# Performance work log

Measured on AMD Instinct MI355X. Metric: run time of the kernel, lower is better.

Reference implementation:

```python
import jax, jax.numpy as jnp
import numpy as np

N_NODES, N_EDGES, D_IN, N_GRAPHS = 20000, 320000, 256, 32
H1, C1, H2, C2 = 4, 128, 4, 64


def setup_inputs() -> dict:
    key = jax.random.key(0)
    ks = jax.random.split(key, 24)
    g = lambda k, shape, fan: jax.random.normal(k, shape, jnp.float32) * (1.0 / np.sqrt(fan))
    inp = {
        'x': jax.random.normal(ks[0], (N_NODES, D_IN), jnp.float32),
        'edge_index': jax.random.randint(ks[1], (2, N_EDGES), 0, N_NODES, jnp.int32),
        'batch': jnp.sort(jax.random.randint(ks[2], (N_NODES,), 0, N_GRAPHS, jnp.int32)),
        'edge_attr': jax.random.normal(ks[3], (N_EDGES, 1), jnp.float32),
        # GATConv 1: lin [D_IN, H1*C1], att_src/dst/edge [H1,C1], lin_edge [1,H1*C1], bias [H1*C1]
        'W1': g(ks[4], (D_IN, H1 * C1), D_IN),
        'as1': g(ks[5], (H1, C1), C1),
        'ad1': g(ks[6], (H1, C1), C1),
        'We1': g(ks[7], (1, H1 * C1), 1),
        'ae1': g(ks[8], (H1, C1), C1),
        'b1': jnp.zeros((H1 * C1,), jnp.float32),
        'g1': jnp.ones((H1 * C1,), jnp.float32),
        'be1': jnp.zeros((H1 * C1,), jnp.float32),
        # GATConv 2 (concat=False -> out 64)
        'W2': g(ks[9], (H1 * C1, H2 * C2), H1 * C1),
        'as2': g(ks[10], (H2, C2), C2),
        'ad2': g(ks[11], (H2, C2), C2),
        'We2': g(ks[12], (1, H2 * C2), 1),
        'ae2': g(ks[13], (H2, C2), C2),
        'b2': jnp.zeros((C2,), jnp.float32),
        'g2': jnp.ones((C2,), jnp.float32),
        'be2': jnp.zeros((C2,), jnp.float32),
        'fw1': g(ks[14], (C2, 32), C2),
        'fb1': jnp.zeros((32,), jnp.float32),
        'fw2': g(ks[15], (32, 1), 32),
        'fb2': jnp.zeros((1,), jnp.float32),
    }
    return inp


def _gat(x, src, dst, ea, W, a_s, a_d, We, a_e, bias, H, C, concat, n):
    h = (x @ W).reshape(n, H, C)                         # [N,H,C]
    al_s = jnp.einsum('nhc,hc->nh', h, a_s)              # [N,H]
    al_d = jnp.einsum('nhc,hc->nh', h, a_d)
    e = (ea @ We).reshape(-1, H, C)                      # [E',H,C]
    al_e = jnp.einsum('ehc,hc->eh', e, a_e)
    logits = jax.nn.leaky_relu(al_s[src] + al_d[dst] + al_e, 0.2)  # [E',H]
    m = jax.ops.segment_max(logits, dst, num_segments=n)
    m = jnp.where(jnp.isfinite(m), m, 0.0)
    p = jnp.exp(logits - m[dst])
    denom = jax.ops.segment_sum(p, dst, num_segments=n)
    alpha = p / (denom[dst] + 1e-16)                     # segment softmax
    out = jax.ops.segment_sum(h[src] * alpha[:, :, None], dst, num_segments=n)
    out = out.reshape(n, H * C) if concat else out.mean(axis=1)
    return out + bias


def _bn(x, gamma, beta):
    mu = x.mean(axis=0)
    var = x.var(axis=0)
    return gamma * (x - mu) * jax.lax.rsqrt(var + 1e-5) + beta


def reference(x, edge_index, batch, edge_attr, W1, as1, ad1, We1, ae1, b1, g1, be1,
              W2, as2, ad2, We2, ae2, b2, g2, be2, fw1, fb1, fw2, fb2):
    n = x.shape[0]
    loop = jnp.arange(n, dtype=edge_index.dtype)
    src = jnp.concatenate([edge_index[0], loop])
    dst = jnp.concatenate([edge_index[1], loop])
    # self-loop edge_attr filled with mean (PyG fill_value='mean')
    ea = jnp.concatenate([edge_attr, jnp.broadcast_to(edge_attr.mean(axis=0), (n, edge_attr.shape[1]))])

    h = _gat(x, src, dst, ea, W1, as1, ad1, We1, ae1, b1, H1, C1, True, n)
    h = jax.nn.elu(_bn(h, g1, be1))
    h = _gat(h, src, dst, ea, W2, as2, ad2, We2, ae2, b2, H2, C2, False, n)
    h = jax.nn.elu(_bn(h, g2, be2))

    sums = jax.ops.segment_sum(h, batch, num_segments=N_GRAPHS)
    cnt = jax.ops.segment_sum(jnp.ones((n,), h.dtype), batch, num_segments=N_GRAPHS)
    pooled = sums / jnp.maximum(cnt, 1.0)[:, None]       # global_mean_pool
    # dropout is identity in eval mode
    out = jax.nn.elu(pooled @ fw1 + fb1) @ fw2 + fb2
    return out
```

## Files before the change

kernel.cpp:

```cpp
#include <hip/hip_runtime.h>
#include <hip/hip_bf16.h>

#define N_NODES  20000
#define MPAD     20096
#define N_EDGES  320000
#define N_EP     (N_EDGES + N_NODES)
#define D_IN     256
#define N_GRAPHS 32
#define HH1 4
#define CC1 128
#define HH2 4
#define CC2 64
#define MAXDEG   128

#define XB_OFF      0ull
#define HB1_OFF     10289152ull
#define AGG1_OFF    30867456ull
#define HB2_OFF     51445760ull
#define OUT2_OFF    61734912ull
#define EAF_OFF     66854912ull
#define W1BT_OFF    68134912ull
#define W2BT_OFF    68397056ull
#define CSR_OFF     68659200ull
#define ROWPTR_OFF  71379200ull
#define GSTART_OFF  71459264ull
#define SMALL_OFF   71459520ull
#define SBUF_OFF    71485120ull
#define EAP_OFF     71485184ull
#define ALSP_OFF    71486464ull
#define ALDP_OFF    72129536ull
#define PMU1_OFF    72772608ull
#define PM21_OFF    73296896ull
#define PMU2_OFF    73821184ull
#define PM22_OFF    73886720ull
#define A1_OFF      73952256ull
#define B1_OFF      73954304ull
#define A2_OFF      73956352ull
#define B2_OFF      73956608ull
#define EAACC_OFF   73956864ull
#define ALS_OFF     73956928ull
#define ALD_OFF     74278464ull
#define DEG_OFF     74600000ull
#define CURS_OFF    74680000ull
#define FLAGZ_OFF   74760000ull
#define ZERO0_START DEG_OFF
#define ZERO0_SIZE  160128ull
#define PP_OFF      74760128ull

#define S_AS1 0
#define S_AD1 512
#define S_WE1 1024
#define S_AE1 1536
#define S_G1  2048
#define S_BE1 2560
#define S_AS2 3072
#define S_AD2 3328
#define S_WE2 3584
#define S_AE2 3840
#define S_G2  4096
#define S_BE2 4160
#define S_FW1 4224
#define S_FB1 6272
#define S_FW2 6304
#define S_FB2 6336

typedef __attribute__((ext_vector_type(8))) short bf8_t;
typedef __attribute__((ext_vector_type(4))) float f4_t;

__global__ void detect_dtype(const unsigned short* __restrict__ xr, int* __restrict__ flag) {
    int i = blockIdx.x * blockDim.x + threadIdx.x;
    unsigned short u = xr[i];
    if ((u & 0x7F80) == 0x7F80) atomicOr(flag, 1);
}

__device__ __forceinline__ float loadF(const void* p, int i, int fp32) {
    return fp32 ? ((const float*)p)[i]
                : __bfloat162float(((const __hip_bfloat16*)p)[i]);
}

#define PB_XB  5024
#define PB_EAF 313
#define PB_W   512
#define PB_SM  16
#define PREP_BLOCKS (PB_XB + PB_EAF + 2 * PB_W + PB_SM + 1)
__global__ __launch_bounds__(256) void prep(
        const int* __restrict__ flag,
        const void* x, const void* ea, const void* W1, const void* W2,
        const void* as1, const void* ad1, const void* We1, const void* ae1,
        const void* g1, const void* be1, const void* as2, const void* ad2,
        const void* We2, const void* ae2, const void* g2, const void* be2,
        const void* fw1, const void* fb1, const void* fw2, const void* fb2,
        __hip_bfloat16* __restrict__ xb, float* __restrict__ eaf, float* __restrict__ eap,
        __hip_bfloat16* __restrict__ W1bt, __hip_bfloat16* __restrict__ W2bt,
        float* __restrict__ smalls, float* __restrict__ sbuf) {
    __shared__ float sh[256];
    int b = blockIdx.x, t = threadIdx.x;
    int fp32 = flag[0];
    if (b < PB_XB) {
        int base = (b * 256 + t) * 4;
        __hip_bfloat16 tmp[4];
#pragma unroll
        for (int j = 0; j < 4; ++j) {
            int i = base + j;
            float v = (i < N_NODES * D_IN) ? loadF(x, i, fp32) : 0.f;
            tmp[j] = __float2bfloat16(v);
        }
        *(uint2*)&xb[base] = *(uint2*)tmp;
        return;
    }
    b -= PB_XB;
    if (b < PB_EAF) {
        int base = (b * 256 + t) * 4;
        float s = 0.f;
#pragma unroll
        for (int j = 0; j < 4; ++j) {
            int i = base + j;
            if (i < N_EDGES) { float v = loadF(ea, i, fp32); eaf[i] = v; s += v; }
        }
        sh[t] = s;
        __syncthreads();
        for (int st = 128; st; st >>= 1) {
            if (t < st) sh[t] += sh[t + st];
            __syncthreads();
        }
        if (t == 0) eap[b] = sh[0];
        return;
    }
    b -= PB_EAF;
    if (b < PB_W) {
        int i = b * 256 + t;
        int k = i >> 9, n = i & 511;
        W1bt[(size_t)n * 256 + k] = __float2bfloat16(loadF(W1, i, fp32));
        return;
    }
    b -= PB_W;
    if (b < PB_W) {
        int i = b * 256 + t;
        int k = i >> 8, n = i & 255;
        W2bt[(size_t)n * 512 + k] = __float2bfloat16(loadF(W2, i, fp32));
        return;
    }
    b -= PB_W;
    if (b < PB_SM) {
        const void* srcs[16] = {as1, ad1, We1, ae1, g1, be1, as2, ad2, We2, ae2, g2, be2, fw1, fb1, fw2, fb2};
        const int cnts[16] = {512, 512, 512, 512, 512, 512, 256, 256, 256, 256, 64, 64, 2048, 32, 32, 1};
        const int offs[16] = {S_AS1, S_AD1, S_WE1, S_AE1, S_G1, S_BE1, S_AS2, S_AD2,
                              S_WE2, S_AE2, S_G2, S_BE2, S_FW1, S_FB1, S_FW2, S_FB2};
        for (int i = t; i < cnts[b]; i += 256)
            smalls[offs[b] + i] = loadF(srcs[b], i, fp32);
        return;
    }
    if (t < 4) {
        float s = 0.f;
        for (int c = 0; c < CC1; ++c) s += loadF(We1, t * CC1 + c, fp32) * loadF(ae1, t * CC1 + c, fp32);
        sbuf[t] = s;
    } else if (t < 8) {
        int h = t - 4;
        float s = 0.f;
        for (int c = 0; c < CC2; ++c) s += loadF(We2, h * CC2 + c, fp32) * loadF(ae2, h * CC2 + c, fp32);
        sbuf[4 + h] = s;
    }
}

#define HIST_BLOCKS 1329
__global__ void hist_bounds(const int* __restrict__ ei, int* __restrict__ deg,
                            const int* __restrict__ batch, int* __restrict__ gstart) {
    int b = blockIdx.x, t = threadIdx.x;
    if (b < HIST_BLOCKS) {
        int e = b * 256 + t;
        if (e >= N_EP) return;
        int d = (e < N_EDGES) ? ei[N_EDGES + e] : e - N_EDGES;
        atomicAdd(&deg[d], 1);
        return;
    }
    int i = (b - HIST_BLOCKS) * 256 + t;
    if (i >= N_NODES) return;
    int bb = batch[i];
    if (i == 0) {
        for (int g = 0; g <= bb; ++g) gstart[g] = 0;
    } else {
        int pb = batch[i - 1];
        for (int g = pb + 1; g <= bb; ++g) gstart[g] = i;
    }
    if (i == N_NODES - 1) {
        for (int g = bb + 1; g <= N_GRAPHS; ++g) gstart[g] = N_NODES;
    }
}

__global__ __launch_bounds__(1024) void deg_scan(const int* __restrict__ deg, int* __restrict__ rowptr,
                                                 const float* __restrict__ eap, float* __restrict__ ea_acc) {
    __shared__ int part[1024];
    int t = threadIdx.x;
    int lo = t * 20;
    int hi = lo + 20; if (hi > N_NODES) hi = N_NODES; if (lo > N_NODES) lo = N_NODES;
    int s = 0;
    for (int i = lo; i < hi; ++i) s += deg[i];
    part[t] = s;
    __syncthreads();
    for (int off = 1; off < 1024; off <<= 1) {
        int u = (t >= off) ? part[t - off] : 0;
        __syncthreads();
        if (t >= off) part[t] += u;
        __syncthreads();
    }
    int run = part[t] - s;
    for (int i = lo; i < hi; ++i) { rowptr[i] = run; run += deg[i]; }
    if (hi == N_NODES && lo < N_NODES) rowptr[N_NODES] = run;
    if (t == 0) {
        float es = 0.f;
        for (int i = 0; i < PB_EAF; ++i) es += eap[i];
        ea_acc[0] = es;
    }
}

__global__ void edge_scatter(const int* __restrict__ ei, const int* __restrict__ rowptr,
                             int* __restrict__ cursor, int2* __restrict__ csr_se) {
    int e = blockIdx.x * blockDim.x + threadIdx.x;
    if (e >= N_EP) return;
    int s, d;
    if (e < N_EDGES) { s = ei[e]; d = ei[N_EDGES + e]; }
    else { s = d = e - N_EDGES; }
    int pos = rowptr[d] + atomicAdd(&cursor[d], 1);
    csr_se[pos] = make_int2(s, e);
}

__global__ __launch_bounds__(64) void csr_sort_fill(const int* __restrict__ rowptr, int2* __restrict__ cs,
                                                    const float* __restrict__ eaf,
                                                    const float* __restrict__ ea_acc) {
    __shared__ int2 buf[128];
    int d = blockIdx.x;
    int beg = rowptr[d], end = rowptr[d + 1], n = end - beg;
    int lane = threadIdx.x;
    float ea_mean = ea_acc[0] * (1.0f / N_EDGES);
    if (n <= 0) return;
    if (n <= 128) {
        for (int i = lane; i < n; i += 64) buf[i] = cs[beg + i];
        __syncthreads();
        for (int r = 0; r < n; ++r) {
            int i = 2 * lane + (r & 1);
            if (i + 1 < n) {
                int2 a = buf[i], b = buf[i + 1];
                if (a.y > b.y) { buf[i] = b; buf[i + 1] = a; }
            }
            __syncthreads();
        }
        for (int i = lane; i < n; i += 64) {
            int2 se = buf[i];
            float eav = (se.y < N_EDGES) ? eaf[se.y] : ea_mean;
            se.y = __float_as_int(eav);
            cs[beg + i] = se;
        }
    } else {
        if (lane == 0) {
            for (int i = beg + 1; i < end; ++i) {
                int2 key = cs[i]; int j = i - 1;
                while (j >= beg && cs[j].y > key.y) { cs[j + 1] = cs[j]; --j; }
                cs[j + 1] = key;
            }
        }
        __syncthreads();
        for (int i = lane; i < n; i += 64) {
            int2 se = cs[beg + i];
            float eav = (se.y < N_EDGES) ? eaf[se.y] : ea_mean;
            se.y = __float_as_int(eav);
            cs[beg + i] = se;
        }
    }
}

__global__ __launch_bounds__(256) void gemm_mfma_al(
        const short* __restrict__ A, const short* __restrict__ Bt,
        __hip_bfloat16* __restrict__ Cb, int N, int K,
        float* __restrict__ alsp, float* __restrict__ aldp,
        const float* __restrict__ asv, const float* __restrict__ adv, int cshift) {
    __shared__ short As[128 * 40];
    __shared__ short Bs[64 * 40];
    int t = threadIdx.x;
    int wv = t >> 6, lane = t & 63, quad = lane >> 4, lr = lane & 15;
    int m0 = blockIdx.y * 128, n0 = blockIdx.x * 64;
    f4_t acc[2][4] = {};
    int ra0 = t >> 2, sa0 = t & 3;
    int ra1 = (t + 256) >> 2;
    for (int k0 = 0; k0 < K; k0 += 32) {
        *(uint4*)&As[ra0 * 40 + sa0 * 8] = *(const uint4*)&A[(size_t)(m0 + ra0) * K + k0 + sa0 * 8];
        *(uint4*)&As[ra1 * 40 + sa0 * 8] = *(const uint4*)&A[(size_t)(m0 + ra1) * K + k0 + sa0 * 8];
        *(uint4*)&Bs[ra0 * 40 + sa0 * 8] = *(const uint4*)&Bt[(size_t)(n0 + ra0) * K + k0 + sa0 * 8];
        __syncthreads();
        bf8_t a0 = *(const bf8_t*)&As[(wv * 16 + lr) * 40 + quad * 8];
        bf8_t a1 = *(const bf8_t*)&As[((wv + 4) * 16 + lr) * 40 + quad * 8];
#pragma unroll
        for (int nt = 0; nt < 4; ++nt) {
            bf8_t b = *(const bf8_t*)&Bs[(nt * 16 + lr) * 40 + quad * 8];
            acc[0][nt] = __builtin_amdgcn_mfma_f32_16x16x32_bf16(a0, b, acc[0][nt], 0, 0, 0);
            acc[1][nt] = __builtin_amdgcn_mfma_f32_16x16x32_bf16(a1, b, acc[1][nt], 0, 0, 0);
        }
        __syncthreads();
    }
#pragma unroll
    for (int si = 0; si < 2; ++si) {
        int mrow = m0 + (wv + si * 4) * 16 + quad * 4;
#pragma unroll
        for (int nt = 0; nt < 4; ++nt) {
            int col = n0 + nt * 16 + lr;
#pragma unroll
            for (int r = 0; r < 4; ++r)
                Cb[(size_t)(mrow + r) * N + col] = __float2bfloat16(acc[si][nt][r]);
        }
    }
    float asv4[4], adv4[4];
#pragma unroll
    for (int nt = 0; nt < 4; ++nt) {
        asv4[nt] = asv[n0 + nt * 16 + lr];
        adv4[nt] = adv[n0 + nt * 16 + lr];
    }
    int hsel = n0 >> cshift;
    int parity = (n0 >> 6) & ((1 << (cshift - 6)) - 1);
#pragma unroll
    for (int si = 0; si < 2; ++si) {
#pragma unroll
        for (int r = 0; r < 4; ++r) {
            float ps = 0.f, pd = 0.f;
#pragma unroll
            for (int nt = 0; nt < 4; ++nt) {
                ps += acc[si][nt][r] * asv4[nt];
                pd += acc[si][nt][r] * adv4[nt];
            }
#pragma unroll
            for (int m = 1; m < 16; m <<= 1) {
                ps += __shfl_xor(ps, m);
                pd += __shfl_xor(pd, m);
            }
            if (lr == 0) {
                int row = m0 + (wv + si * 4) * 16 + quad * 4 + r;
                alsp[(row * 4 + hsel) * 2 + parity] = ps;
                aldp[(row * 4 + hsel) * 2 + parity] = pd;
            }
        }
    }
}

__global__ void al_combine(const float* __restrict__ alsp, const float* __restrict__ aldp,
                           float* __restrict__ als, float* __restrict__ ald, int nparts) {
    int i = blockIdx.x * blockDim.x + threadIdx.x;
    if (i >= MPAD * 4) return;
    float s = alsp[2 * i], d0 = aldp[2 * i];
    if (nparts == 2) { s += alsp[2 * i + 1]; d0 += aldp[2 * i + 1]; }
    als[i] = s; ald[i] = d0;
}

__global__ __launch_bounds__(128) void fused_agg1(
        const int* __restrict__ rowptr, const int2* __restrict__ cs,
        const float* __restrict__ als, const float* __restrict__ ald,
        const float* __restrict__ sbuf, const __hip_bfloat16* __restrict__ hb,
        __hip_bfloat16* __restrict__ outb) {
    __shared__ float lg[2][MAXDEG * 4];
    __shared__ int   ssrc[2][MAXDEG];
    int wv = threadIdx.x >> 6, t = threadIdx.x & 63;
    int d = blockIdx.x * 2 + wv;
    int beg = rowptr[d], n = rowptr[d + 1] - beg;
    bool fit = (n <= MAXDEG);
    float4 adv = *(const float4*)&ald[d * 4];
    float adh[4] = {adv.x, adv.y, adv.z, adv.w};
    float sb4[4] = {sbuf[0], sbuf[1], sbuf[2], sbuf[3]};
    float mx[4] = {-INFINITY, -INFINITY, -INFINITY, -INFINITY};
    for (int p = t; p < n; p += 64) {
        int2 se = cs[beg + p];
        float eav = __int_as_float(se.y);
        float4 as = *(const float4*)&als[se.x * 4];
        float l[4] = {as.x, as.y, as.z, as.w};
#pragma unroll
        for (int hh = 0; hh < 4; ++hh) {
            float v = l[hh] + adh[hh] + eav * sb4[hh];
            v = v > 0.f ? v : 0.2f * v;
            l[hh] = v;
            mx[hh] = fmaxf(mx[hh], v);
        }
        if (fit) {
            *(float4*)&lg[wv][p * 4] = make_float4(l[0], l[1], l[2], l[3]);
            ssrc[wv][p] = se.x;
        }
    }
#pragma unroll
    for (int m = 1; m < 64; m <<= 1)
#pragma unroll
        for (int hh = 0; hh < 4; ++hh)
            mx[hh] = fmaxf(mx[hh], __shfl_xor(mx[hh], m));
    asm volatile("s_waitcnt lgkmcnt(0)" ::: "memory");
    int h = t >> 4;
    float mh = mx[h];
    float a[8] = {};
    float ds = 0.f;
    const __hip_bfloat16* hrow = hb + 8 * t;
#define ACC8(rr, wt) { \
    unsigned q0 = (rr).x, q1 = (rr).y, q2 = (rr).z, q3 = (rr).w; \
    a[0] += (wt) * __uint_as_float(q0 << 16); a[1] += (wt) * __uint_as_float(q0 & 0xFFFF0000u); \
    a[2] += (wt) * __uint_as_float(q1 << 16); a[3] += (wt) * __uint_as_float(q1 & 0xFFFF0000u); \
    a[4] += (wt) * __uint_as_float(q2 << 16); a[5] += (wt) * __uint_as_float(q2 & 0xFFFF0000u); \
    a[6] += (wt) * __uint_as_float(q3 << 16); a[7] += (wt) * __uint_as_float(q3 & 0xFFFF0000u); }
    if (fit) {
        int p = 0;
        for (; p + 8 <= n; p += 8) {
            int s0 = ssrc[wv][p],     s1 = ssrc[wv][p + 1], s2 = ssrc[wv][p + 2], s3 = ssrc[wv][p + 3];
            int s4 = ssrc[wv][p + 4], s5 = ssrc[wv][p + 5], s6 = ssrc[wv][p + 6], s7 = ssrc[wv][p + 7];
            uint4 r0 = *(const uint4*)&hrow[(size_t)s0 * 512];
            uint4 r1 = *(const uint4*)&hrow[(size_t)s1 * 512];
            uint4 r2 = *(const uint4*)&hrow[(size_t)s2 * 512];
            uint4 r3 = *(const uint4*)&hrow[(size_t)s3 * 512];
            uint4 r4 = *(const uint4*)&hrow[(size_t)s4 * 512];
            uint4 r5 = *(const uint4*)&hrow[(size_t)s5 * 512];
            uint4 r6 = *(const uint4*)&hrow[(size_t)s6 * 512];
            uint4 r7 = *(const uint4*)&hrow[(size_t)s7 * 512];
            float w0 = __expf(lg[wv][p * 4 + h] - mh);
            float w1 = __expf(lg[wv][p * 4 + 4 + h] - mh);
            float w2 = __expf(lg[wv][p * 4 + 8 + h] - mh);
            float w3 = __expf(lg[wv][p * 4 + 12 + h] - mh);
            float w4 = __expf(lg[wv][p * 4 + 16 + h] - mh);
            float w5 = __expf(lg[wv][p * 4 + 20 + h] - mh);
            float w6 = __expf(lg[wv][p * 4 + 24 + h] - mh);
            float w7 = __expf(lg[wv][p * 4 + 28 + h] - mh);
            ds += ((w0 + w1) + (w2 + w3)) + ((w4 + w5) + (w6 + w7));
            ACC8(r0, w0); ACC8(r1, w1); ACC8(r2, w2); ACC8(r3, w3);
            ACC8(r4, w4); ACC8(r5, w5); ACC8(r6, w6); ACC8(r7, w7);
        }
        for (; p + 4 <= n; p += 4) {
            int s0 = ssrc[wv][p], s1 = ssrc[wv][p + 1], s2 = ssrc[wv][p + 2], s3 = ssrc[wv][p + 3];
            uint4 r0 = *(const uint4*)&hrow[(size_t)s0 * 512];
            uint4 r1 = *(const uint4*)&hrow[(size_t)s1 * 512];
            uint4 r2 = *(const uint4*)&hrow[(size_t)s2 * 512];
            uint4 r3 = *(const uint4*)&hrow[(size_t)s3 * 512];
            float w0 = __expf(lg[wv][p * 4 + h] - mh);
            float w1 = __expf(lg[wv][p * 4 + 4 + h] - mh);
            float w2 = __expf(lg[wv][p * 4 + 8 + h] - mh);
            float w3 = __expf(lg[wv][p * 4 + 12 + h] - mh);
            ds += (w0 + w1) + (w2 + w3);
            ACC8(r0, w0); ACC8(r1, w1); ACC8(r2, w2); ACC8(r3, w3);
        }
        for (; p < n; ++p) {
            int s0 = ssrc[wv][p];
            uint4 r0 = *(const uint4*)&hrow[(size_t)s0 * 512];
            float w0 = __expf(lg[wv][p * 4 + h] - mh);
            ds += w0;
            ACC8(r0, w0);
        }
    } else {
        for (int p = 0; p < n; ++p) {
            int2 se = cs[beg + p];
            float eav = __int_as_float(se.y);
            float l = als[se.x * 4 + h] + adh[h] + eav * sb4[h];
            l = l > 0.f ? l : 0.2f * l;
            float w = __expf(l - mh);
            uint4 r0 = *(const uint4*)&hrow[(size_t)se.x * 512];
            ds += w;
            ACC8(r0, w);
        }
    }
#undef ACC8
    float rdn = 1.0f / (ds + 1e-16f);
    __hip_bfloat16 tmp[8];
#pragma unroll
    for (int j = 0; j < 8; ++j) tmp[j] = __float2bfloat16(a[j] * rdn);
    *(uint4*)&outb[(size_t)d * 512 + 8 * t] = *(uint4*)tmp;
}

__global__ __launch_bounds__(128) void fused_agg2(
        const int* __restrict__ rowptr, const int2* __restrict__ cs,
        const float* __restrict__ als, const float* __restrict__ ald,
        const float* __restrict__ sbuf, const __hip_bfloat16* __restrict__ hb,
        float* __restrict__ out2) {
    __shared__ float lg[2][MAXDEG * 4];
    __shared__ int   ssrc[2][MAXDEG];
    int wv = threadIdx.x >> 6, t = threadIdx.x & 63;
    int d = blockIdx.x * 2 + wv;
    int beg = rowptr[d], n = rowptr[d + 1] - beg;
    bool fit = (n <= MAXDEG);
    float4 adv = *(const float4*)&ald[d * 4];
    float adh[4] = {adv.x, adv.y, adv.z, adv.w};
    float sb4[4] = {sbuf[4], sbuf[5], sbuf[6], sbuf[7]};
    float mx[4] = {-INFINITY, -INFINITY, -INFINITY, -INFINITY};
    for (int p = t; p < n; p += 64) {
        int2 se = cs[beg + p];
        float eav = __int_as_float(se.y);
        float4 as = *(const float4*)&als[se.x * 4];
        float l[4] = {as.x, as.y, as.z, as.w};
#pragma unroll
        for (int hh = 0; hh < 4; ++hh) {
            float v = l[hh] + adh[hh] + eav * sb4[hh];
            v = v > 0.f ? v : 0.2f * v;
            l[hh] = v;
            mx[hh] = fmaxf(mx[hh], v);
        }
        if (fit) {
            *(float4*)&lg[wv][p * 4] = make_float4(l[0], l[1], l[2], l[3]);
            ssrc[wv][p] = se.x;
        }
    }
#pragma unroll
    for (int m = 1; m < 64; m <<= 1)
#pragma unroll
        for (int hh = 0; hh < 4; ++hh)
            mx[hh] = fmaxf(mx[hh], __shfl_xor(mx[hh], m));
    asm volatile("s_waitcnt lgkmcnt(0)" ::: "memory");
    int h = t >> 4;
    float mh = mx[h];
    float a4[4] = {};
    float ds = 0.f;
    const __hip_bfloat16* hrow = hb + 4 * t;
#define ACC4(rr, wt) { \
    unsigned q0 = (rr).x, q1 = (rr).y; \
    a4[0] += (wt) * __uint_as_float(q0 << 16); a4[1] += (wt) * __uint_as_float(q0 & 0xFFFF0000u); \
    a4[2] += (wt) * __uint_as_float(q1 << 16); a4[3] += (wt) * __uint_as_float(q1 & 0xFFFF0000u); }
    if (fit) {
        int p = 0;
        for (; p + 8 <= n; p += 8) {
            int s0 = ssrc[wv][p],     s1 = ssrc[wv][p + 1], s2 = ssrc[wv][p + 2], s3 = ssrc[wv][p + 3];
            int s4 = ssrc[wv][p + 4], s5 = ssrc[wv][p + 5], s6 = ssrc[wv][p + 6], s7 = ssrc[wv][p + 7];
            uint2 r0 = *(const uint2*)&hrow[(size_t)s0 * 256];
            uint2 r1 = *(const uint2*)&hrow[(size_t)s1 * 256];
            uint2 r2 = *(const uint2*)&hrow[(size_t)s2 * 256];
            uint2 r3 = *(const uint2*)&hrow[(size_t)s3 * 256];
            uint2 r4 = *(const uint2*)&hrow[(size_t)s4 * 256];
            uint2 r5 = *(const uint2*)&hrow[(size_t)s5 * 256];
            uint2 r6 = *(const uint2*)&hrow[(size_t)s6 * 256];
            uint2 r7 = *(const uint2*)&hrow[(size_t)s7 * 256];
            float w0 = __expf(lg[wv][p * 4 + h] - mh);
            float w1 = __expf(lg[wv][p * 4 + 4 + h] - mh);
            float w2 = __expf(lg[wv][p * 4 + 8 + h] - mh);
            float w3 = __expf(lg[wv][p * 4 + 12 + h] - mh);
            float w4 = __expf(lg[wv][p * 4 + 16 + h] - mh);
            float w5 = __expf(lg[wv][p * 4 + 20 + h] - mh);
            float w6 = __expf(lg[wv][p * 4 + 24 + h] - mh);
            float w7 = __expf(lg[wv][p * 4 + 28 + h] - mh);
            ds += ((w0 + w1) + (w2 + w3)) + ((w4 + w5) + (w6 + w7));
            ACC4(r0, w0); ACC4(r1, w1); ACC4(r2, w2); ACC4(r3, w3);
            ACC4(r4, w4); ACC4(r5, w5); ACC4(r6, w6); ACC4(r7, w7);
        }
        for (; p + 4 <= n; p += 4) {
            int s0 = ssrc[wv][p], s1 = ssrc[wv][p + 1], s2 = ssrc[wv][p + 2], s3 = ssrc[wv][p + 3];
            uint2 r0 = *(const uint2*)&hrow[(size_t)s0 * 256];
            uint2 r1 = *(const uint2*)&hrow[(size_t)s1 * 256];
            uint2 r2 = *(const uint2*)&hrow[(size_t)s2 * 256];
            uint2 r3 = *(const uint2*)&hrow[(size_t)s3 * 256];
            float w0 = __expf(lg[wv][p * 4 + h] - mh);
            float w1 = __expf(lg[wv][p * 4 + 4 + h] - mh);
            float w2 = __expf(lg[wv][p * 4 + 8 + h] - mh);
            float w3 = __expf(lg[wv][p * 4 + 12 + h] - mh);
            ds += (w0 + w1) + (w2 + w3);
            ACC4(r0, w0); ACC4(r1, w1); ACC4(r2, w2); ACC4(r3, w3);
        }
        for (; p < n; ++p) {
            int s0 = ssrc[wv][p];
            uint2 r0 = *(const uint2*)&hrow[(size_t)s0 * 256];
            float w0 = __expf(lg[wv][p * 4 + h] - mh);
            ds += w0;
            ACC4(r0, w0);
        }
    } else {
        for (int p = 0; p < n; ++p) {
            int2 se = cs[beg + p];
            float eav = __int_as_float(se.y);
            float l = als[se.x * 4 + h] + adh[h] + eav * sb4[h];
            l = l > 0.f ? l : 0.2f * l;
            float w = __expf(l - mh);
            uint2 r0 = *(const uint2*)&hrow[(size_t)se.x * 256];
            ds += w;
            ACC4(r0, w);
        }
    }
#undef ACC4
    float rdn = 1.0f / (ds + 1e-16f);
#pragma unroll
    for (int j = 0; j < 4; ++j) {
        float v = a4[j] * rdn;
        v += __shfl_xor(v, 16);
        v += __shfl_xor(v, 32);
        a4[j] = v * 0.25f;
    }
    if (t < 16)
        *(float4*)&out2[(size_t)d * 64 + 4 * t] = make_float4(a4[0], a4[1], a4[2], a4[3]);
}

__global__ __launch_bounds__(256) void bn_part_b(const __hip_bfloat16* __restrict__ x,
                                                 float* __restrict__ pmu, float* __restrict__ pm2) {
    int t = threadIdx.x, b = blockIdx.x;
    float s0 = 0.f, s20 = 0.f, s1 = 0.f, s21 = 0.f;
    for (int i = b; i < N_NODES; i += gridDim.x) {
        unsigned u = *(const unsigned*)&x[(size_t)i * 512 + 2 * t];
        float v0 = __uint_as_float(u << 16);
        float v1 = __uint_as_float(u & 0xFFFF0000u);
        s0 += v0; s20 += v0 * v0; s1 += v1; s21 += v1 * v1;
    }
    pmu[b * 512 + 2 * t] = s0;     pm2[b * 512 + 2 * t] = s20;
    pmu[b * 512 + 2 * t + 1] = s1; pm2[b * 512 + 2 * t + 1] = s21;
}

__global__ void bn_reduce_affine(const float* __restrict__ pmu, const float* __restrict__ pm2,
                                 const float* __restrict__ smalls, int s_g, int s_be,
                                 float* __restrict__ a, float* __restrict__ b, int nch) {
    int c = blockIdx.x * blockDim.x + threadIdx.x;
    if (c >= nch) return;
    float s = 0.f, s2 = 0.f;
    for (int bk = 0; bk < 256; ++bk) { s += pmu[bk * nch + c]; s2 += pm2[bk * nch + c]; }
    float m = s * (1.0f / N_NODES);
    float var = s2 * (1.0f / N_NODES) - m * m;
    float aa = smalls[s_g + c] * rsqrtf(var + 1e-5f);
    a[c] = aa;
    b[c] = smalls[s_be + c] - m * aa;
}

__global__ __launch_bounds__(256) void bn_apply_elu_b16(__hip_bfloat16* __restrict__ x,
                                                        const float* __restrict__ a,
                                                        const float* __restrict__ b) {
    int q = blockIdx.x * blockDim.x + threadIdx.x;
    if (q >= N_NODES * 512 / 4) return;
    int base = q * 4;
    int j = base & 511;
    uint2 raw = *(uint2*)&x[base];
    float v[4] = {__uint_as_float(raw.x << 16), __uint_as_float(raw.x & 0xFFFF0000u),
                  __uint_as_float(raw.y << 16), __uint_as_float(raw.y & 0xFFFF0000u)};
    __hip_bfloat16 tmp[4];
#pragma unroll
    for (int k = 0; k < 4; ++k) {
        float y = a[j + k] * v[k] + b[j + k];
        y = y > 0.f ? y : expm1f(y);
        tmp[k] = __float2bfloat16(y);
    }
    *(uint2*)&x[base] = *(uint2*)tmp;
}

__global__ __launch_bounds__(256) void bn2_stats(const float* __restrict__ x,
                                                 float* __restrict__ pmu, float* __restrict__ pm2) {
    int t = threadIdx.x;
    int c = t & 63, j = t >> 6;
    float ls = 0.f, ls2 = 0.f;
    for (int nd = blockIdx.x * 4 + j; nd < N_NODES; nd += gridDim.x * 4) {
        float v = x[(size_t)nd * 64 + c];
        ls += v; ls2 += v * v;
    }
    __shared__ float shs[4][64], sh2[4][64];
    shs[j][c] = ls; sh2[j][c] = ls2;
    __syncthreads();
    if (j == 0) {
        pmu[blockIdx.x * 64 + c] = shs[0][c] + shs[1][c] + shs[2][c] + shs[3][c];
        pm2[blockIdx.x * 64 + c] = sh2[0][c] + sh2[1][c] + sh2[2][c] + sh2[3][c];
    }
}

__global__ __launch_bounds__(256) void pool_part(const float* __restrict__ x, const int* __restrict__ gstart,
                                                 const float* __restrict__ a2, const float* __restrict__ b2,
                                                 float* __restrict__ pp) {
    int g = blockIdx.x >> 3, ck = blockIdx.x & 7;
    int t = threadIdx.x;
    int c = t & 63, j = t >> 6;
    int beg = gstart[g], end = gstart[g + 1], n = end - beg;
    int cb = beg + (n * ck) / 8, ce = beg + (n * (ck + 1)) / 8;
    float ac = a2[c], bc = b2[c];
    float s = 0.f;
    for (int i = cb + j; i < ce; i += 4) {
        float y = ac * x[(size_t)i * 64 + c] + bc;
        s += (y > 0.f ? y : expm1f(y));
    }
    __shared__ float sh[4][64];
    sh[j][c] = s;
    __syncthreads();
    if (j == 0)
        pp[blockIdx.x * 64 + c] = sh[0][c] + sh[1][c] + sh[2][c] + sh[3][c];
}

__global__ __launch_bounds__(64) void pool_mlp_fin(const float* __restrict__ pp, const int* __restrict__ gstart,
                                                   const float* __restrict__ smalls, const int* __restrict__ flag,
                                                   void* __restrict__ outp) {
    int g = blockIdx.x, t = threadIdx.x;
    __shared__ float pooled[64];
    __shared__ float hsh[32];
    float s = 0.f;
    for (int k = 0; k < 8; ++k) s += pp[(g * 8 + k) * 64 + t];
    int n = gstart[g + 1] - gstart[g];
    pooled[t] = s / fmaxf((float)n, 1.0f);
    __syncthreads();
    if (t < 32) {
        float acc = smalls[S_FB1 + t];
        for (int cc = 0; cc < 64; ++cc)
            acc += pooled[cc] * smalls[S_FW1 + cc * 32 + t];
        hsh[t] = acc > 0.f ? acc : expm1f(acc);
    }
    __syncthreads();
    if (t == 0) {
        float o = smalls[S_FB2];
        for (int k = 0; k < 32; ++k) o += hsh[k] * smalls[S_FW2 + k];
        if (flag[0]) ((float*)outp)[g] = o;
        else ((__hip_bfloat16*)outp)[g] = __float2bfloat16(o);
    }
}

extern "C" void kernel_launch(void* const* d_in, const int* in_sizes, int n_in,
                              void* d_out, int out_size, void* d_ws, size_t ws_size,
                              hipStream_t stream) {
    const void* x    = d_in[0];
    const int* ei    = (const int*)d_in[1];
    const int* batch = (const int*)d_in[2];
    const void* ea   = d_in[3];
    const void* W1   = d_in[4];
    const void* as1  = d_in[5];
    const void* ad1  = d_in[6];
    const void* We1  = d_in[7];
    const void* ae1  = d_in[8];
    const void* g1   = d_in[10];
    const void* be1  = d_in[11];
    const void* W2   = d_in[12];
    const void* as2  = d_in[13];
    const void* ad2  = d_in[14];
    const void* We2  = d_in[15];
    const void* ae2  = d_in[16];
    const void* g2   = d_in[18];
    const void* be2  = d_in[19];
    const void* fw1  = d_in[20];
    const void* fb1  = d_in[21];
    const void* fw2  = d_in[22];
    const void* fb2  = d_in[23];

    char* ws = (char*)d_ws;
    __hip_bfloat16* xb   = (__hip_bfloat16*)(ws + XB_OFF);
    __hip_bfloat16* hb1  = (__hip_bfloat16*)(ws + HB1_OFF);
    __hip_bfloat16* agg1 = (__hip_bfloat16*)(ws + AGG1_OFF);
    __hip_bfloat16* hb2  = (__hip_bfloat16*)(ws + HB2_OFF);
    float* out2   = (float*)(ws + OUT2_OFF);
    float* eaf    = (float*)(ws + EAF_OFF);
    __hip_bfloat16* W1bt = (__hip_bfloat16*)(ws + W1BT_OFF);
    __hip_bfloat16* W2bt = (__hip_bfloat16*)(ws + W2BT_OFF);
    int2*  csr_se = (int2*)(ws + CSR_OFF);
    int*   rowptr = (int*)(ws + ROWPTR_OFF);
    int*   gstart = (int*)(ws + GSTART_OFF);
    float* smalls = (float*)(ws + SMALL_OFF);
    float* sbuf   = (float*)(ws + SBUF_OFF);
    float* eap    = (float*)(ws + EAP_OFF);
    float* alsp   = (float*)(ws + ALSP_OFF);
    float* aldp   = (float*)(ws + ALDP_OFF);
    float* pmu1   = (float*)(ws + PMU1_OFF);
    float* pm21   = (float*)(ws + PM21_OFF);
    float* pmu2   = (float*)(ws + PMU2_OFF);
    float* pm22   = (float*)(ws + PM22_OFF);
    float* a1     = (float*)(ws + A1_OFF);
    float* b1     = (float*)(ws + B1_OFF);
    float* a2     = (float*)(ws + A2_OFF);
    float* b2     = (float*)(ws + B2_OFF);
    float* ea_acc = (float*)(ws + EAACC_OFF);
    float* als    = (float*)(ws + ALS_OFF);
    float* ald    = (float*)(ws + ALD_OFF);
    float* pp     = (float*)(ws + PP_OFF);
    int*   deg    = (int*)(ws + DEG_OFF);
    int*   cursor = (int*)(ws + CURS_OFF);
    int*   flag   = (int*)(ws + FLAGZ_OFF);

    hipMemsetAsync(ws + ZERO0_START, 0, ZERO0_SIZE, stream);

    detect_dtype<<<256, 256, 0, stream>>>((const unsigned short*)x, flag);
    prep<<<PREP_BLOCKS, 256, 0, stream>>>(flag, x, ea, W1, W2,
                                          as1, ad1, We1, ae1, g1, be1, as2, ad2,
                                          We2, ae2, g2, be2, fw1, fb1, fw2, fb2,
                                          xb, eaf, eap, W1bt, W2bt, smalls, sbuf);

    hist_bounds<<<HIST_BLOCKS + 79, 256, 0, stream>>>(ei, deg, batch, gstart);
    deg_scan<<<1, 1024, 0, stream>>>(deg, rowptr, eap, ea_acc);
    edge_scatter<<<HIST_BLOCKS, 256, 0, stream>>>(ei, rowptr, cursor, csr_se);
    csr_sort_fill<<<N_NODES, 64, 0, stream>>>(rowptr, csr_se, eaf, ea_acc);

    gemm_mfma_al<<<dim3(512 / 64, MPAD / 128), 256, 0, stream>>>(
        (const short*)xb, (const short*)W1bt, hb1, 512, 256,
        alsp, aldp, smalls + S_AS1, smalls + S_AD1, 7);
    al_combine<<<(MPAD * 4 + 255) / 256, 256, 0, stream>>>(alsp, aldp, als, ald, 2);
    fused_agg1<<<N_NODES / 2, 128, 0, stream>>>(rowptr, csr_se, als, ald, sbuf, hb1, agg1);
    bn_part_b<<<256, 256, 0, stream>>>(agg1, pmu1, pm21);
    bn_reduce_affine<<<2, 256, 0, stream>>>(pmu1, pm21, smalls, S_G1, S_BE1, a1, b1, 512);
    bn_apply_elu_b16<<<10000, 256, 0, stream>>>(agg1, a1, b1);

    gemm_mfma_al<<<dim3(256 / 64, MPAD / 128), 256, 0, stream>>>(
        (const short*)agg1, (const short*)W2bt, hb2, 256, 512,
        alsp, aldp, smalls + S_AS2, smalls + S_AD2, 6);
    al_combine<<<(MPAD * 4 + 255) / 256, 256, 0, stream>>>(alsp, aldp, als, ald, 1);
    fused_agg2<<<N_NODES / 2, 128, 0, stream>>>(rowptr, csr_se, als, ald, sbuf, hb2, out2);
    bn2_stats<<<256, 256, 0, stream>>>(out2, pmu2, pm22);
    bn_reduce_affine<<<1, 64, 0, stream>>>(pmu2, pm22, smalls, S_G2, S_BE2, a2, b2, 64);

    pool_part<<<N_GRAPHS * 8, 256, 0, stream>>>(out2, gstart, a2, b2, pp);
    pool_mlp_fin<<<N_GRAPHS, 64, 0, stream>>>(pp, gstart, smalls, flag, d_out);
}
```

Before: 420.7 us.

## Drop al_combine via atomics, merge pooling kernels, widen aggregation blocks

The GEMM epilogue now adds the per-head attention partial sums straight into zeroed als/ald buffers with atomics, which removes the al_combine kernels and their partial-sum buffers. The memset region grows to cover the new buffers. The two pooling kernels become one per-graph kernel, and the aggregation kernels handle four nodes per 256-thread block instead of two. The ea-mean sum in deg_scan becomes a parallel tree reduction. Risks: float atomics make the result order-dependent and nondeterministic, and pooling now runs on only 32 blocks.

```diff
diff --git a/kernel.cpp b/kernel.cpp
--- a/kernel.cpp
+++ b/kernel.cpp
@@ -27,8 +27,6 @@
 #define SMALL_OFF   71459520ull
 #define SBUF_OFF    71485120ull
 #define EAP_OFF     71485184ull
-#define ALSP_OFF    71486464ull
-#define ALDP_OFF    72129536ull
 #define PMU1_OFF    72772608ull
 #define PM21_OFF    73296896ull
 #define PMU2_OFF    73821184ull
@@ -38,14 +36,16 @@
 #define A2_OFF      73956352ull
 #define B2_OFF      73956608ull
 #define EAACC_OFF   73956864ull
-#define ALS_OFF     73956928ull
-#define ALD_OFF     74278464ull
 #define DEG_OFF     74600000ull
 #define CURS_OFF    74680000ull
 #define FLAGZ_OFF   74760000ull
+#define PP_OFF      74760128ull
+#define ALS1_OFF    74825664ull
+#define ALD1_OFF    75147200ull
+#define ALS2_OFF    75468736ull
+#define ALD2_OFF    75790272ull
 #define ZERO0_START DEG_OFF
-#define ZERO0_SIZE  160128ull
-#define PP_OFF      74760128ull
+#define ZERO0_SIZE  1511808ull
 
 #define S_AS1 0
 #define S_AD1 512
@@ -190,6 +190,7 @@
 __global__ __launch_bounds__(1024) void deg_scan(const int* __restrict__ deg, int* __restrict__ rowptr,
                                                  const float* __restrict__ eap, float* __restrict__ ea_acc) {
     __shared__ int part[1024];
+    __shared__ float fsh[512];
     int t = threadIdx.x;
     int lo = t * 20;
     int hi = lo + 20; if (hi > N_NODES) hi = N_NODES; if (lo > N_NODES) lo = N_NODES;
@@ -206,11 +207,13 @@
     int run = part[t] - s;
     for (int i = lo; i < hi; ++i) { rowptr[i] = run; run += deg[i]; }
     if (hi == N_NODES && lo < N_NODES) rowptr[N_NODES] = run;
-    if (t == 0) {
-        float es = 0.f;
-        for (int i = 0; i < PB_EAF; ++i) es += eap[i];
-        ea_acc[0] = es;
-    }
+    if (t < 512) fsh[t] = (t < PB_EAF) ? eap[t] : 0.f;
+    __syncthreads();
+    for (int st = 256; st; st >>= 1) {
+        if (t < st) fsh[t] += fsh[t + st];
+        __syncthreads();
+    }
+    if (t == 0) ea_acc[0] = fsh[0];
 }
 
 __global__ void edge_scatter(const int* __restrict__ ei, const int* __restrict__ rowptr,
@@ -271,7 +274,7 @@
 __global__ __launch_bounds__(256) void gemm_mfma_al(
         const short* __restrict__ A, const short* __restrict__ Bt,
         __hip_bfloat16* __restrict__ Cb, int N, int K,
-        float* __restrict__ alsp, float* __restrict__ aldp,
+        float* __restrict__ als, float* __restrict__ ald,
         const float* __restrict__ asv, const float* __restrict__ adv, int cshift) {
     __shared__ short As[128 * 40];
     __shared__ short Bs[64 * 40];
@@ -314,7 +317,6 @@
         adv4[nt] = adv[n0 + nt * 16 + lr];
     }
     int hsel = n0 >> cshift;
-    int parity = (n0 >> 6) & ((1 << (cshift - 6)) - 1);
 #pragma unroll
     for (int si = 0; si < 2; ++si) {
 #pragma unroll
@@ -332,31 +334,22 @@
             }
             if (lr == 0) {
                 int row = m0 + (wv + si * 4) * 16 + quad * 4 + r;
-                alsp[(row * 4 + hsel) * 2 + parity] = ps;
-                aldp[(row * 4 + hsel) * 2 + parity] = pd;
+                atomicAdd(&als[row * 4 + hsel], ps);
+                atomicAdd(&ald[row * 4 + hsel], pd);
             }
         }
     }
 }
 
-__global__ void al_combine(const float* __restrict__ alsp, const float* __restrict__ aldp,
-                           float* __restrict__ als, float* __restrict__ ald, int nparts) {
-    int i = blockIdx.x * blockDim.x + threadIdx.x;
-    if (i >= MPAD * 4) return;
-    float s = alsp[2 * i], d0 = aldp[2 * i];
-    if (nparts == 2) { s += alsp[2 * i + 1]; d0 += aldp[2 * i + 1]; }
-    als[i] = s; ald[i] = d0;
-}
-
-__global__ __launch_bounds__(128) void fused_agg1(
+__global__ __launch_bounds__(256) void fused_agg1(
         const int* __restrict__ rowptr, const int2* __restrict__ cs,
         const float* __restrict__ als, const float* __restrict__ ald,
         const float* __restrict__ sbuf, const __hip_bfloat16* __restrict__ hb,
         __hip_bfloat16* __restrict__ outb) {
-    __shared__ float lg[2][MAXDEG * 4];
-    __shared__ int   ssrc[2][MAXDEG];
+    __shared__ float lg[4][MAXDEG * 4];
+    __shared__ int   ssrc[4][MAXDEG];
     int wv = threadIdx.x >> 6, t = threadIdx.x & 63;
-    int d = blockIdx.x * 2 + wv;
+    int d = blockIdx.x * 4 + wv;
     int beg = rowptr[d], n = rowptr[d + 1] - beg;
     bool fit = (n <= MAXDEG);
     float4 adv = *(const float4*)&ald[d * 4];
@@ -462,15 +455,15 @@
     *(uint4*)&outb[(size_t)d * 512 + 8 * t] = *(uint4*)tmp;
 }
 
-__global__ __launch_bounds__(128) void fused_agg2(
+__global__ __launch_bounds__(256) void fused_agg2(
         const int* __restrict__ rowptr, const int2* __restrict__ cs,
         const float* __restrict__ als, const float* __restrict__ ald,
         const float* __restrict__ sbuf, const __hip_bfloat16* __restrict__ hb,
         float* __restrict__ out2) {
-    __shared__ float lg[2][MAXDEG * 4];
-    __shared__ int   ssrc[2][MAXDEG];
+    __shared__ float lg[4][MAXDEG * 4];
+    __shared__ int   ssrc[4][MAXDEG];
     int wv = threadIdx.x >> 6, t = threadIdx.x & 63;
-    int d = blockIdx.x * 2 + wv;
+    int d = blockIdx.x * 4 + wv;
     int beg = rowptr[d], n = rowptr[d + 1] - beg;
     bool fit = (n <= MAXDEG);
     float4 adv = *(const float4*)&ald[d * 4];
@@ -645,37 +638,28 @@
     }
 }
 
-__global__ __launch_bounds__(256) void pool_part(const float* __restrict__ x, const int* __restrict__ gstart,
-                                                 const float* __restrict__ a2, const float* __restrict__ b2,
-                                                 float* __restrict__ pp) {
-    int g = blockIdx.x >> 3, ck = blockIdx.x & 7;
-    int t = threadIdx.x;
+__global__ __launch_bounds__(256) void pool_mlp(const float* __restrict__ x, const int* __restrict__ gstart,
+                                                const float* __restrict__ a2, const float* __restrict__ b2,
+                                                const float* __restrict__ smalls, const int* __restrict__ flag,
+                                                void* __restrict__ outp) {
+    int g = blockIdx.x, t = threadIdx.x;
     int c = t & 63, j = t >> 6;
-    int beg = gstart[g], end = gstart[g + 1], n = end - beg;
-    int cb = beg + (n * ck) / 8, ce = beg + (n * (ck + 1)) / 8;
+    int beg = gstart[g], end = gstart[g + 1];
     float ac = a2[c], bc = b2[c];
     float s = 0.f;
-    for (int i = cb + j; i < ce; i += 4) {
+    for (int i = beg + j; i < end; i += 4) {
         float y = ac * x[(size_t)i * 64 + c] + bc;
         s += (y > 0.f ? y : expm1f(y));
     }
     __shared__ float sh[4][64];
+    __shared__ float pooled[64];
+    __shared__ float hsh[32];
     sh[j][c] = s;
     __syncthreads();
-    if (j == 0)
-        pp[blockIdx.x * 64 + c] = sh[0][c] + sh[1][c] + sh[2][c] + sh[3][c];
-}
-
-__global__ __launch_bounds__(64) void pool_mlp_fin(const float* __restrict__ pp, const int* __restrict__ gstart,
-                                                   const float* __restrict__ smalls, const int* __restrict__ flag,
-                                                   void* __restrict__ outp) {
-    int g = blockIdx.x, t = threadIdx.x;
-    __shared__ float pooled[64];
-    __shared__ float hsh[32];
-    float s = 0.f;
-    for (int k = 0; k < 8; ++k) s += pp[(g * 8 + k) * 64 + t];
-    int n = gstart[g + 1] - gstart[g];
-    pooled[t] = s / fmaxf((float)n, 1.0f);
+    if (t < 64) {
+        int n = end - beg;
+        pooled[t] = (sh[0][t] + sh[1][t] + sh[2][t] + sh[3][t]) / fmaxf((float)n, 1.0f);
+    }
     __syncthreads();
     if (t < 32) {
         float acc = smalls[S_FB1 + t];
@@ -733,8 +717,6 @@
     float* smalls = (float*)(ws + SMALL_OFF);
     float* sbuf   = (float*)(ws + SBUF_OFF);
     float* eap    = (float*)(ws + EAP_OFF);
-    float* alsp   = (float*)(ws + ALSP_OFF);
-    float* aldp   = (float*)(ws + ALDP_OFF);
     float* pmu1   = (float*)(ws + PMU1_OFF);
     float* pm21   = (float*)(ws + PM21_OFF);
     float* pmu2   = (float*)(ws + PMU2_OFF);
@@ -744,9 +726,10 @@
     float* a2     = (float*)(ws + A2_OFF);
     float* b2     = (float*)(ws + B2_OFF);
     float* ea_acc = (float*)(ws + EAACC_OFF);
-    float* als    = (float*)(ws + ALS_OFF);
-    float* ald    = (float*)(ws + ALD_OFF);
-    float* pp     = (float*)(ws + PP_OFF);
+    float* als1   = (float*)(ws + ALS1_OFF);
+    float* ald1   = (float*)(ws + ALD1_OFF);
+    float* als2   = (float*)(ws + ALS2_OFF);
+    float* ald2   = (float*)(ws + ALD2_OFF);
     int*   deg    = (int*)(ws + DEG_OFF);
     int*   cursor = (int*)(ws + CURS_OFF);
     int*   flag   = (int*)(ws + FLAGZ_OFF);
@@ -766,21 +749,18 @@
 
     gemm_mfma_al<<<dim3(512 / 64, MPAD / 128), 256, 0, stream>>>(
         (const short*)xb, (const short*)W1bt, hb1, 512, 256,
-        alsp, aldp, smalls + S_AS1, smalls + S_AD1, 7);
-    al_combine<<<(MPAD * 4 + 255) / 256, 256, 0, stream>>>(alsp, aldp, als, ald, 2);
-    fused_agg1<<<N_NODES / 2, 128, 0, stream>>>(rowptr, csr_se, als, ald, sbuf, hb1, agg1);
+        als1, ald1, smalls + S_AS1, smalls + S_AD1, 7);
+    fused_agg1<<<N_NODES / 4, 256, 0, stream>>>(rowptr, csr_se, als1, ald1, sbuf, hb1, agg1);
     bn_part_b<<<256, 256, 0, stream>>>(agg1, pmu1, pm21);
     bn_reduce_affine<<<2, 256, 0, stream>>>(pmu1, pm21, smalls, S_G1, S_BE1, a1, b1, 512);
     bn_apply_elu_b16<<<10000, 256, 0, stream>>>(agg1, a1, b1);
 
     gemm_mfma_al<<<dim3(256 / 64, MPAD / 128), 256, 0, stream>>>(
         (const short*)agg1, (const short*)W2bt, hb2, 256, 512,
-        alsp, aldp, smalls + S_AS2, smalls + S_AD2, 6);
-    al_combine<<<(MPAD * 4 + 255) / 256, 256, 0, stream>>>(alsp, aldp, als, ald, 1);
-    fused_agg2<<<N_NODES / 2, 128, 0, stream>>>(rowptr, csr_se, als, ald, sbuf, hb2, out2);
+        als2, ald2, smalls + S_AS2, smalls + S_AD2, 6);
+    fused_agg2<<<N_NODES / 4, 256, 0, stream>>>(rowptr, csr_se, als2, ald2, sbuf, hb2, out2);
     bn2_stats<<<256, 256, 0, stream>>>(out2, pmu2, pm22);
     bn_reduce_affine<<<1, 64, 0, stream>>>(pmu2, pm22, smalls, S_G2, S_BE2, a2, b2, 64);
 
-    pool_part<<<N_GRAPHS * 8, 256, 0, stream>>>(out2, gstart, a2, b2, pp);
-    pool_mlp_fin<<<N_GRAPHS, 64, 0, stream>>>(pp, gstart, smalls, flag, d_out);
-}
+    pool_mlp<<<N_GRAPHS, 256, 0, stream>>>(out2, gstart, a2, b2, smalls, flag, d_out);
+}
```

Measured after the change: 477.5 us. +13.5%, slower.

## Merge dtype detect with histogram, parallelise small reductions and register-sort short rows

Applied to the files above, without the earlier changes.

Folds dtype detection into the histogram/graph-bounds kernel to save a launch, and replaces the serial eap summation in deg_scan with a shared-memory tree reduction. The prep block reduction now uses wavefront shuffles, and bn_reduce_affine splits its 256-block partial-sum loop across four waves. csr_sort_fill gains a register-resident odd-even transposition sort for rows of at most 64 edges, avoiding LDS round trips and barriers. These remove serial latency on small preprocessing steps; the in-register sort still runs n rounds of two shuffles each.

```diff
diff --git a/kernel.cpp b/kernel.cpp
--- a/kernel.cpp
+++ b/kernel.cpp
@@ -67,15 +67,43 @@
 typedef __attribute__((ext_vector_type(8))) short bf8_t;
 typedef __attribute__((ext_vector_type(4))) float f4_t;
 
-__global__ void detect_dtype(const unsigned short* __restrict__ xr, int* __restrict__ flag) {
-    int i = blockIdx.x * blockDim.x + threadIdx.x;
-    unsigned short u = xr[i];
-    if ((u & 0x7F80) == 0x7F80) atomicOr(flag, 1);
-}
-
 __device__ __forceinline__ float loadF(const void* p, int i, int fp32) {
     return fp32 ? ((const float*)p)[i]
                 : __bfloat162float(((const __hip_bfloat16*)p)[i]);
+}
+
+#define DH_DETECT 256
+#define HIST_BLOCKS 1329
+__global__ void detect_hist(const unsigned short* __restrict__ xr, int* __restrict__ flag,
+                            const int* __restrict__ ei, int* __restrict__ deg,
+                            const int* __restrict__ batch, int* __restrict__ gstart) {
+    int b = blockIdx.x, t = threadIdx.x;
+    if (b < DH_DETECT) {
+        int i = b * 256 + t;
+        unsigned short u = xr[i];
+        if ((u & 0x7F80) == 0x7F80) atomicOr(flag, 1);
+        return;
+    }
+    b -= DH_DETECT;
+    if (b < HIST_BLOCKS) {
+        int e = b * 256 + t;
+        if (e >= N_EP) return;
+        int d = (e < N_EDGES) ? ei[N_EDGES + e] : e - N_EDGES;
+        atomicAdd(&deg[d], 1);
+        return;
+    }
+    int i = (b - HIST_BLOCKS) * 256 + t;
+    if (i >= N_NODES) return;
+    int bb = batch[i];
+    if (i == 0) {
+        for (int g = 0; g <= bb; ++g) gstart[g] = 0;
+    } else {
+        int pb = batch[i - 1];
+        for (int g = pb + 1; g <= bb; ++g) gstart[g] = i;
+    }
+    if (i == N_NODES - 1) {
+        for (int g = bb + 1; g <= N_GRAPHS; ++g) gstart[g] = N_NODES;
+    }
 }
 
 #define PB_XB  5024
@@ -93,7 +121,7 @@
         __hip_bfloat16* __restrict__ xb, float* __restrict__ eaf, float* __restrict__ eap,
         __hip_bfloat16* __restrict__ W1bt, __hip_bfloat16* __restrict__ W2bt,
         float* __restrict__ smalls, float* __restrict__ sbuf) {
-    __shared__ float sh[256];
+    __shared__ float shw[4];
     int b = blockIdx.x, t = threadIdx.x;
     int fp32 = flag[0];
     if (b < PB_XB) {
@@ -117,13 +145,11 @@
             int i = base + j;
             if (i < N_EDGES) { float v = loadF(ea, i, fp32); eaf[i] = v; s += v; }
         }
-        sh[t] = s;
+#pragma unroll
+        for (int m = 1; m < 64; m <<= 1) s += __shfl_xor(s, m);
+        if ((t & 63) == 0) shw[t >> 6] = s;
         __syncthreads();
-        for (int st = 128; st; st >>= 1) {
-            if (t < st) sh[t] += sh[t + st];
-            __syncthreads();
-        }
-        if (t == 0) eap[b] = sh[0];
+        if (t == 0) eap[b] = shw[0] + shw[1] + shw[2] + shw[3];
         return;
     }
     b -= PB_EAF;
@@ -162,34 +188,10 @@
     }
 }
 
-#define HIST_BLOCKS 1329
-__global__ void hist_bounds(const int* __restrict__ ei, int* __restrict__ deg,
-                            const int* __restrict__ batch, int* __restrict__ gstart) {
-    int b = blockIdx.x, t = threadIdx.x;
-    if (b < HIST_BLOCKS) {
-        int e = b * 256 + t;
-        if (e >= N_EP) return;
-        int d = (e < N_EDGES) ? ei[N_EDGES + e] : e - N_EDGES;
-        atomicAdd(&deg[d], 1);
-        return;
-    }
-    int i = (b - HIST_BLOCKS) * 256 + t;
-    if (i >= N_NODES) return;
-    int bb = batch[i];
-    if (i == 0) {
-        for (int g = 0; g <= bb; ++g) gstart[g] = 0;
-    } else {
-        int pb = batch[i - 1];
-        for (int g = pb + 1; g <= bb; ++g) gstart[g] = i;
-    }
-    if (i == N_NODES - 1) {
-        for (int g = bb + 1; g <= N_GRAPHS; ++g) gstart[g] = N_NODES;
-    }
-}
-
 __global__ __launch_bounds__(1024) void deg_scan(const int* __restrict__ deg, int* __restrict__ rowptr,
                                                  const float* __restrict__ eap, float* __restrict__ ea_acc) {
     __shared__ int part[1024];
+    __shared__ float fsh[512];
     int t = threadIdx.x;
     int lo = t * 20;
     int hi = lo + 20; if (hi > N_NODES) hi = N_NODES; if (lo > N_NODES) lo = N_NODES;
@@ -206,11 +208,13 @@
     int run = part[t] - s;
     for (int i = lo; i < hi; ++i) { rowptr[i] = run; run += deg[i]; }
     if (hi == N_NODES && lo < N_NODES) rowptr[N_NODES] = run;
-    if (t == 0) {
-        float es = 0.f;
-        for (int i = 0; i < PB_EAF; ++i) es += eap[i];
-        ea_acc[0] = es;
-    }
+    if (t < 512) fsh[t] = (t < PB_EAF) ? eap[t] : 0.f;
+    __syncthreads();
+    for (int st = 256; st; st >>= 1) {
+        if (t < st) fsh[t] += fsh[t + st];
+        __syncthreads();
+    }
+    if (t == 0) ea_acc[0] = fsh[0];
 }
 
 __global__ void edge_scatter(const int* __restrict__ ei, const int* __restrict__ rowptr,
@@ -233,6 +237,24 @@
     int lane = threadIdx.x;
     float ea_mean = ea_acc[0] * (1.0f / N_EDGES);
     if (n <= 0) return;
+    if (n <= 64) {
+        int key = 0x7FFFFFFF, val = 0;
+        if (lane < n) { int2 se = cs[beg + lane]; key = se.y; val = se.x; }
+        for (int r = 0; r < n; ++r) {
+            bool up = ((lane & 1) == (r & 1));
+            int partner = up ? lane + 1 : lane - 1;
+            bool valid = (partner >= 0) && (partner < 64);
+            int pidx = valid ? partner : lane;
+            int pk = __shfl(key, pidx);
+            int pv = __shfl(val, pidx);
+            if (valid && (up ? (pk < key) : (pk > key))) { key = pk; val = pv; }
+        }
+        if (lane < n) {
+            float eav = (key < N_EDGES) ? eaf[key] : ea_mean;
+            cs[beg + lane] = make_int2(val, __float_as_int(eav));
+        }
+        return;
+    }
     if (n <= 128) {
         for (int i = lane; i < n; i += 64) buf[i] = cs[beg + i];
         __syncthreads();
@@ -250,21 +272,21 @@
             se.y = __float_as_int(eav);
             cs[beg + i] = se;
         }
-    } else {
-        if (lane == 0) {
-            for (int i = beg + 1; i < end; ++i) {
-                int2 key = cs[i]; int j = i - 1;
-                while (j >= beg && cs[j].y > key.y) { cs[j + 1] = cs[j]; --j; }
-                cs[j + 1] = key;
-            }
-        }
-        __syncthreads();
-        for (int i = lane; i < n; i += 64) {
-            int2 se = cs[beg + i];
-            float eav = (se.y < N_EDGES) ? eaf[se.y] : ea_mean;
-            se.y = __float_as_int(eav);
-            cs[beg + i] = se;
-        }
+        return;
+    }
+    if (lane == 0) {
+        for (int i = beg + 1; i < end; ++i) {
+            int2 key = cs[i]; int j = i - 1;
+            while (j >= beg && cs[j].y > key.y) { cs[j + 1] = cs[j]; --j; }
+            cs[j + 1] = key;
+        }
+    }
+    __syncthreads();
+    for (int i = lane; i < n; i += 64) {
+        int2 se = cs[beg + i];
+        float eav = (se.y < N_EDGES) ? eaf[se.y] : ea_mean;
+        se.y = __float_as_int(eav);
+        cs[beg + i] = se;
     }
 }
 
@@ -593,18 +615,26 @@
     pmu[b * 512 + 2 * t + 1] = s1; pm2[b * 512 + 2 * t + 1] = s21;
 }
 
-__global__ void bn_reduce_affine(const float* __restrict__ pmu, const float* __restrict__ pm2,
+__global__ __launch_bounds__(256) void bn_reduce_affine(const float* __restrict__ pmu, const float* __restrict__ pm2,
                                  const float* __restrict__ smalls, int s_g, int s_be,
                                  float* __restrict__ a, float* __restrict__ b, int nch) {
-    int c = blockIdx.x * blockDim.x + threadIdx.x;
-    if (c >= nch) return;
+    __shared__ float shs[4][64], sh2[4][64];
+    int t = threadIdx.x;
+    int cl = t & 63, j = t >> 6;
+    int c = blockIdx.x * 64 + cl;
     float s = 0.f, s2 = 0.f;
-    for (int bk = 0; bk < 256; ++bk) { s += pmu[bk * nch + c]; s2 += pm2[bk * nch + c]; }
-    float m = s * (1.0f / N_NODES);
-    float var = s2 * (1.0f / N_NODES) - m * m;
-    float aa = smalls[s_g + c] * rsqrtf(var + 1e-5f);
-    a[c] = aa;
-    b[c] = smalls[s_be + c] - m * aa;
+    for (int bk = j * 64; bk < (j + 1) * 64; ++bk) { s += pmu[bk * nch + c]; s2 += pm2[bk * nch + c]; }
+    shs[j][cl] = s; sh2[j][cl] = s2;
+    __syncthreads();
+    if (j == 0) {
+        float st  = ((shs[0][cl] + shs[1][cl]) + (shs[2][cl] + shs[3][cl]));
+        float st2 = ((sh2[0][cl] + sh2[1][cl]) + (sh2[2][cl] + sh2[3][cl]));
+        float m = st * (1.0f / N_NODES);
+        float var = st2 * (1.0f / N_NODES) - m * m;
+        float aa = smalls[s_g + c] * rsqrtf(var + 1e-5f);
+        a[c] = aa;
+        b[c] = smalls[s_be + c] - m * aa;
+    }
 }
 
 __global__ __launch_bounds__(256) void bn_apply_elu_b16(__hip_bfloat16* __restrict__ x,
@@ -753,13 +783,13 @@
 
     hipMemsetAsync(ws + ZERO0_START, 0, ZERO0_SIZE, stream);
 
-    detect_dtype<<<256, 256, 0, stream>>>((const unsigned short*)x, flag);
+    detect_hist<<<DH_DETECT + HIST_BLOCKS + 79, 256, 0, stream>>>(
+        (const unsigned short*)x, flag, ei, deg, batch, gstart);
     prep<<<PREP_BLOCKS, 256, 0, stream>>>(flag, x, ea, W1, W2,
                                           as1, ad1, We1, ae1, g1, be1, as2, ad2,
                                           We2, ae2, g2, be2, fw1, fb1, fw2, fb2,
                                           xb, eaf, eap, W1bt, W2bt, smalls, sbuf);
 
-    hist_bounds<<<HIST_BLOCKS + 79, 256, 0, stream>>>(ei, deg, batch, gstart);
     deg_scan<<<1, 1024, 0, stream>>>(deg, rowptr, eap, ea_acc);
     edge_scatter<<<HIST_BLOCKS, 256, 0, stream>>>(ei, rowptr, cursor, csr_se);
     csr_sort_fill<<<N_NODES, 64, 0, stream>>>(rowptr, csr_se, eaf, ea_acc);
@@ -770,7 +800,7 @@
     al_combine<<<(MPAD * 4 + 255) / 256, 256, 0, stream>>>(alsp, aldp, als, ald, 2);
     fused_agg1<<<N_NODES / 2, 128, 0, stream>>>(rowptr, csr_se, als, ald, sbuf, hb1, agg1);
     bn_part_b<<<256, 256, 0, stream>>>(agg1, pmu1, pm21);
-    bn_reduce_affine<<<2, 256, 0, stream>>>(pmu1, pm21, smalls, S_G1, S_BE1, a1, b1, 512);
+    bn_reduce_affine<<<8, 256, 0, stream>>>(pmu1, pm21, smalls, S_G1, S_BE1, a1, b1, 512);
     bn_apply_elu_b16<<<10000, 256, 0, stream>>>(agg1, a1, b1);
 
     gemm_mfma_al<<<dim3(256 / 64, MPAD / 128), 256, 0, stream>>>(
@@ -779,7 +809,7 @@
     al_combine<<<(MPAD * 4 + 255) / 256, 256, 0, stream>>>(alsp, aldp, als, ald, 1);
     fused_agg2<<<N_NODES / 2, 128, 0, stream>>>(rowptr, csr_se, als, ald, sbuf, hb2, out2);
     bn2_stats<<<256, 256, 0, stream>>>(out2, pmu2, pm22);
-    bn_reduce_affine<<<1, 64, 0, stream>>>(pmu2, pm22, smalls, S_G2, S_BE2, a2, b2, 64);
+    bn_reduce_affine<<<1, 256, 0, stream>>>(pmu2, pm22, smalls, S_G2, S_BE2, a2, b2, 64);
 
     pool_part<<<N_GRAPHS * 8, 256, 0, stream>>>(out2, gstart, a2, b2, pp);
     pool_mlp_fin<<<N_GRAPHS, 64, 0, stream>>>(pp, gstart, smalls, flag, d_out);
```

Result: no change. 427.6 us (+1.6%).
